# Optimization experiments

Hardware: AMD Instinct MI355X
Metric: run time of the kernel (lower is better)

## Reference

```python
import jax, jax.numpy as jnp
import numpy as np

CLIP_MIN = 0.0  # recurrent_clip_min resolved in build() when -1
CLIP_MAX = 1.0  # recurrent_clip_max default when timesteps unknown


def setup_inputs() -> dict:
    key = jax.random.key(0)
    k1, k2, k3 = jax.random.split(key, 3)
    B, T, D, U = 64, 512, 256, 512
    x = jax.random.normal(k1, (B, T, D), dtype=jnp.float32)
    h0 = jnp.zeros((B, U), dtype=jnp.float32)
    W = jax.random.normal(k2, (D, U), dtype=jnp.float32) * (1.0 / np.sqrt(D))
    u = jax.random.uniform(k3, (U,), dtype=jnp.float32)  # uniform in clip range
    b = jnp.zeros((U,), dtype=jnp.float32)
    return {"x": x, "h0": h0, "W": W, "u": u, "b": b}


def reference(x, h0, W, u, b):
    # IndRNN: h_t = relu(x_t @ W + h_{t-1} * u + b), u clipped to [0, 1]
    u_c = jnp.clip(u, CLIP_MIN, CLIP_MAX)
    # One-time input projection for all timesteps: [B,T,U]
    proj = jnp.einsum("btd,du->btu", x, W) + b
    proj_t = jnp.swapaxes(proj, 0, 1)  # [T,B,U] for scan over time

    def step(h, p_t):
        h_new = jax.nn.relu(p_t + h * u_c)
        return h_new, h_new

    _, hs = jax.lax.scan(step, h0, proj_t)  # hs: [T,B,U]
    return jnp.swapaxes(hs, 0, 1)  # [B,T,U]
```

## Files before the change

kernel.cpp:

```cpp
#include <hip/hip_runtime.h>


__device__ __forceinline__ unsigned short f2bf(float f) {
    unsigned int u = __float_as_uint(f);
    unsigned int r = (u + 0x7FFF + ((u >> 16) & 1)) >> 16;
    return (unsigned short)r;
}

typedef __bf16 bf16x8 __attribute__((ext_vector_type(8)));
typedef float f32x4 __attribute__((ext_vector_type(4)));

typedef const unsigned char __attribute__((address_space(1))) gc_t;
typedef unsigned char __attribute__((address_space(3))) lds_t;

__device__ __forceinline__ void gl_lds16(const void* g, void* l) {
    __builtin_amdgcn_global_load_lds((gc_t*)g, (lds_t*)l, 16, 0, 0);
}

__global__ __launch_bounds__(256) void conv_x(
    const float* __restrict__ x, unsigned short* __restrict__ xb, int n4)
{
    int i = blockIdx.x * blockDim.x + threadIdx.x;
    if (i >= n4) return;
    float4 v = *(const float4*)(x + (long)i * 4);
    ushort4 o;
    o.x = f2bf(v.x); o.y = f2bf(v.y); o.z = f2bf(v.z); o.w = f2bf(v.w);
    *(ushort4*)(xb + (long)i * 4) = o;
}

__global__ __launch_bounds__(256) void conv_wt(
    const float* __restrict__ W, unsigned short* __restrict__ Wt, int K, int N)
{
    int idx = blockIdx.x * blockDim.x + threadIdx.x;
    int kq = K >> 2;
    if (idx >= N * kq) return;
    int n = idx / kq;
    int k4 = (idx - n * kq) * 4;
    ushort4 o;
    o.x = f2bf(W[(long)(k4 + 0) * N + n]);
    o.y = f2bf(W[(long)(k4 + 1) * N + n]);
    o.z = f2bf(W[(long)(k4 + 2) * N + n]);
    o.w = f2bf(W[(long)(k4 + 3) * N + n]);
    *(ushort4*)(Wt + (long)n * K + k4) = o;
}

#define TC 64
#define GN 128

__global__ __launch_bounds__(256, 1) void indrnn_fused(
    const unsigned short* __restrict__ xb,
    const unsigned short* __restrict__ wt,
    const float* __restrict__ bias,
    const float* __restrict__ h0,
    const float* __restrict__ uvec,
    float* __restrict__ out,
    int B, int T, int U)
{
    __shared__ char X[2][TC * 512];

    const int tid  = threadIdx.x;
    const int lane = tid & 63;
    const int w    = tid >> 6;
    const int m    = lane & 15;
    const int quad = lane >> 4;
    const int b    = blockIdx.x;
    const int n0   = blockIdx.y * GN;
    const int tq   = (w >> 1) * 32;
    const int cq   = (w & 1) * 64;

    bf16x8 bfr[4][8];
#pragma unroll
    for (int j = 0; j < 4; ++j)
#pragma unroll
        for (int kt = 0; kt < 8; ++kt)
            bfr[j][kt] = *(const bf16x8*)(
                wt + (long)(n0 + cq + j * 16 + m) * 256 + kt * 32 + quad * 8);

    float bb[4];
#pragma unroll
    for (int j = 0; j < 4; ++j) bb[j] = bias[n0 + cq + j * 16 + m];

    float uc = 0.0f, h = 0.0f;
    if (tid < GN) {
        uc = fminf(fmaxf(uvec[n0 + tid], 0.0f), 1.0f);
        h  = h0[(long)b * U + n0 + tid];
    }

    const unsigned short* xrow = xb + (long)b * T * 256;
    const int p  = lane & 31;
    const int hh = lane >> 5;

#pragma unroll
    for (int i = 0; i < 8; ++i) {
        int blk = i * 4 + w;
        int row = blk * 2 + hh;
        int gp  = p ^ (row & 15);
        gl_lds16(xrow + (long)row * 256 + gp * 8, &X[0][blk * 1024]);
    }

    const int nch = T / TC;
    for (int c = 0; c < nch; ++c) {
        char* Xc = X[c & 1];
        asm volatile("s_waitcnt vmcnt(0)" ::: "memory");
        __builtin_amdgcn_sched_barrier(0);
        __syncthreads();

        f32x4 acc[2][4];
#pragma unroll
        for (int i = 0; i < 2; ++i)
#pragma unroll
            for (int j = 0; j < 4; ++j) acc[i][j] = (f32x4){0.f, 0.f, 0.f, 0.f};

#pragma unroll
        for (int kt = 0; kt < 8; ++kt) {
            const int off = (((kt * 4 + quad) ^ m) * 16);
            bf16x8 a0 = *(const bf16x8*)(Xc + (tq + m) * 512 + off);
            bf16x8 a1 = *(const bf16x8*)(Xc + (tq + 16 + m) * 512 + off);
#pragma unroll
            for (int j = 0; j < 4; ++j) {
                acc[0][j] = __builtin_amdgcn_mfma_f32_16x16x32_bf16(
                    a0, bfr[j][kt], acc[0][j], 0, 0, 0);
                acc[1][j] = __builtin_amdgcn_mfma_f32_16x16x32_bf16(
                    a1, bfr[j][kt], acc[1][j], 0, 0, 0);
            }
        }
        __syncthreads();

        float* pf = (float*)Xc;
#pragma unroll
        for (int i = 0; i < 2; ++i)
#pragma unroll
            for (int j = 0; j < 4; ++j)
#pragma unroll
                for (int r = 0; r < 4; ++r) {
                    int tl  = tq + i * 16 + quad * 4 + r;
                    int col = cq + j * 16 + m;
                    int cs  = col ^ (quad << 4);
                    pf[tl * GN + cs] = acc[i][j][r] + bb[j];
                }
        __syncthreads();

        if (c + 1 < nch) {
            char* Xn = X[(c + 1) & 1];
            const unsigned short* gb = xrow + (long)(c + 1) * TC * 256;
#pragma unroll
            for (int i = 0; i < 8; ++i) {
                int blk = i * 4 + w;
                int row = blk * 2 + hh;
                int gp  = p ^ (row & 15);
                gl_lds16(gb + (long)row * 256 + gp * 8, Xn + blk * 1024);
            }
        }

        if (tid < 128) {
            const float* pfr = (const float*)Xc;
            float* og = out + ((long)b * T + c * TC) * U + n0 + tid;
#pragma unroll 8
            for (int t = 0; t < TC; ++t) {
                float pv = pfr[t * GN + (tid ^ (((t >> 2) & 3) << 4))];
                h = fmaxf(fmaf(h, uc, pv), 0.0f);
                og[(long)t * U] = h;
            }
        }
    }
}

#define BM 128
#define BN 128
#define BK 8

__global__ __launch_bounds__(256) void indrnn_gemm_bias(
    const float* __restrict__ A, const float* __restrict__ Bm,
    const float* __restrict__ bias, float* __restrict__ C,
    int M, int N, int K)
{
    __shared__ float As[BK][BM];
    __shared__ float Bs[BK][BN];
    const int tid = threadIdx.x;
    const int row0 = blockIdx.x * BM, col0 = blockIdx.y * BN;
    const int tx = tid & 15, ty = tid >> 4;
    float acc[8][8];
#pragma unroll
    for (int i = 0; i < 8; ++i)
#pragma unroll
        for (int j = 0; j < 8; ++j) acc[i][j] = 0.0f;
    const int am = tid >> 1, ak = (tid & 1) * 4;
    const int bk = tid >> 5, bn = (tid & 31) * 4;
    const float* Aptr = A + (long)(row0 + am) * K + ak;
    const float* Bptr = Bm + (long)bk * N + col0 + bn;
    for (int kt = 0; kt < K; kt += BK) {
        float4 av = *(const float4*)(Aptr + kt);
        float4 bv = *(const float4*)(Bptr + (long)kt * N);
        As[ak + 0][am] = av.x; As[ak + 1][am] = av.y;
        As[ak + 2][am] = av.z; As[ak + 3][am] = av.w;
        *(float4*)&Bs[bk][bn] = bv;
        __syncthreads();
#pragma unroll
        for (int k = 0; k < BK; ++k) {
            float4 a0 = *(const float4*)&As[k][ty * 4];
            float4 a1 = *(const float4*)&As[k][64 + ty * 4];
            float4 b0 = *(const float4*)&Bs[k][tx * 4];
            float4 b1 = *(const float4*)&Bs[k][64 + tx * 4];
            float a[8] = {a0.x, a0.y, a0.z, a0.w, a1.x, a1.y, a1.z, a1.w};
            float bb2[8] = {b0.x, b0.y, b0.z, b0.w, b1.x, b1.y, b1.z, b1.w};
#pragma unroll
            for (int i = 0; i < 8; ++i)
#pragma unroll
                for (int j = 0; j < 8; ++j)
                    acc[i][j] = fmaf(a[i], bb2[j], acc[i][j]);
        }
        __syncthreads();
    }
    float bb[8];
#pragma unroll
    for (int j = 0; j < 4; ++j) {
        bb[j] = bias[col0 + tx * 4 + j];
        bb[j + 4] = bias[col0 + 64 + tx * 4 + j];
    }
#pragma unroll
    for (int i = 0; i < 8; ++i) {
        const int r = (i < 4) ? (ty * 4 + i) : (64 + ty * 4 + (i - 4));
        float* crow = C + (long)(row0 + r) * N + col0;
        float4 v0 = {acc[i][0] + bb[0], acc[i][1] + bb[1], acc[i][2] + bb[2], acc[i][3] + bb[3]};
        float4 v1 = {acc[i][4] + bb[4], acc[i][5] + bb[5], acc[i][6] + bb[6], acc[i][7] + bb[7]};
        *(float4*)(crow + tx * 4) = v0;
        *(float4*)(crow + 64 + tx * 4) = v1;
    }
}

#define SCAN_UNROLL 32

__global__ __launch_bounds__(256) void indrnn_scan(
    float* __restrict__ out, const float* __restrict__ h0,
    const float* __restrict__ u, int B, int T, int U)
{
    const int idx = blockIdx.x * blockDim.x + threadIdx.x;
    if (idx >= B * U) return;
    const int b = idx / U;
    const int un = idx - b * U;
    const float uc = fminf(fmaxf(u[un], 0.0f), 1.0f);
    float h = h0[(long)b * U + un];
    float* p = out + (long)b * T * U + un;
    for (int t = 0; t < T; t += SCAN_UNROLL) {
        float pv[SCAN_UNROLL];
#pragma unroll
        for (int i = 0; i < SCAN_UNROLL; ++i)
            pv[i] = p[(long)(t + i) * U];
#pragma unroll
        for (int i = 0; i < SCAN_UNROLL; ++i) {
            h = fmaxf(fmaf(h, uc, pv[i]), 0.0f);
            pv[i] = h;
        }
#pragma unroll
        for (int i = 0; i < SCAN_UNROLL; ++i)
            p[(long)(t + i) * U] = pv[i];
    }
}

extern "C" void kernel_launch(void* const* d_in, const int* in_sizes, int n_in,
                              void* d_out, int out_size, void* d_ws, size_t ws_size,
                              hipStream_t stream) {
    const float* x  = (const float*)d_in[0];
    const float* h0 = (const float*)d_in[1];
    const float* W  = (const float*)d_in[2];
    const float* u  = (const float*)d_in[3];
    const float* b  = (const float*)d_in[4];
    float* out = (float*)d_out;

    const int U = in_sizes[3];
    const int B = in_sizes[1] / U;
    const int D = in_sizes[2] / U;
    const int T = in_sizes[0] / (B * D);
    const int M = B * T;

    const size_t xb_bytes = (size_t)M * D * sizeof(unsigned short);
    const size_t wt_bytes = (size_t)U * D * sizeof(unsigned short);
    const bool fused_ok = (D == 256) && (U % GN == 0) && (T % TC == 0) &&
                          (ws_size >= xb_bytes + wt_bytes);

    if (fused_ok) {
        unsigned short* xb = (unsigned short*)d_ws;
        unsigned short* wt = (unsigned short*)((char*)d_ws + xb_bytes);

        const int n4 = (M * D) / 4;
        conv_x<<<(n4 + 255) / 256, 256, 0, stream>>>(x, xb, n4);
        const int nwt = U * (D / 4);
        conv_wt<<<(nwt + 255) / 256, 256, 0, stream>>>(W, wt, D, U);

        dim3 g(B, U / GN);
        indrnn_fused<<<g, 256, 0, stream>>>(xb, wt, b, h0, u, out, B, T, U);
    } else {
        dim3 ggrid(M / BM, U / BN);
        indrnn_gemm_bias<<<ggrid, 256, 0, stream>>>(x, W, b, out, M, U, D);
        const int nthreads = B * U;
        indrnn_scan<<<(nthreads + 255) / 256, 256, 0, stream>>>(out, h0, u, B, T, U);
    }
}
```

Before: 122.1 us.

## Fuse fp32-to-bf16 conversion of x into the recurrent kernel's staging loads

Drops the separate conv_x pass that wrote a bf16 copy of x to workspace. The fused kernel now loads fp32 x straight into registers, converts to bf16 and writes the swizzled tile into LDS. The next chunk's loads are issued before the MFMA loop and stored to LDS after it, so they overlap the compute. This removes one kernel launch and a full write plus reread of the bf16 x buffer. In exchange the kernel reads twice the bytes of x, holds 64 extra registers of prefetch data, and loses the async global-to-LDS path.

```diff
diff --git a/kernel.cpp b/kernel.cpp
--- a/kernel.cpp
+++ b/kernel.cpp
@@ -8,25 +8,8 @@
 }
 
 typedef __bf16 bf16x8 __attribute__((ext_vector_type(8)));
+typedef unsigned short u16x8 __attribute__((ext_vector_type(8)));
 typedef float f32x4 __attribute__((ext_vector_type(4)));
-
-typedef const unsigned char __attribute__((address_space(1))) gc_t;
-typedef unsigned char __attribute__((address_space(3))) lds_t;
-
-__device__ __forceinline__ void gl_lds16(const void* g, void* l) {
-    __builtin_amdgcn_global_load_lds((gc_t*)g, (lds_t*)l, 16, 0, 0);
-}
-
-__global__ __launch_bounds__(256) void conv_x(
-    const float* __restrict__ x, unsigned short* __restrict__ xb, int n4)
-{
-    int i = blockIdx.x * blockDim.x + threadIdx.x;
-    if (i >= n4) return;
-    float4 v = *(const float4*)(x + (long)i * 4);
-    ushort4 o;
-    o.x = f2bf(v.x); o.y = f2bf(v.y); o.z = f2bf(v.z); o.w = f2bf(v.w);
-    *(ushort4*)(xb + (long)i * 4) = o;
-}
 
 __global__ __launch_bounds__(256) void conv_wt(
     const float* __restrict__ W, unsigned short* __restrict__ Wt, int K, int N)
@@ -48,7 +31,7 @@
 #define GN 128
 
 __global__ __launch_bounds__(256, 1) void indrnn_fused(
-    const unsigned short* __restrict__ xb,
+    const float* __restrict__ x,
     const unsigned short* __restrict__ wt,
     const float* __restrict__ bias,
     const float* __restrict__ h0,
@@ -86,24 +69,48 @@
         h  = h0[(long)b * U + n0 + tid];
     }
 
-    const unsigned short* xrow = xb + (long)b * T * 256;
-    const int p  = lane & 31;
-    const int hh = lane >> 5;
-
-#pragma unroll
-    for (int i = 0; i < 8; ++i) {
-        int blk = i * 4 + w;
-        int row = blk * 2 + hh;
-        int gp  = p ^ (row & 15);
-        gl_lds16(xrow + (long)row * 256 + gp * 8, &X[0][blk * 1024]);
+    const float* xbase = x + (long)b * T * 256;
+
+    const int srow = tid >> 5;
+    const int spos = tid & 31;
+
+    {
+        float4 ra[8], rb[8];
+#pragma unroll
+        for (int i = 0; i < 8; ++i) {
+            const float* g = xbase + (srow + 8 * i) * 256 + spos * 8;
+            ra[i] = *(const float4*)g;
+            rb[i] = *(const float4*)(g + 4);
+        }
+#pragma unroll
+        for (int i = 0; i < 8; ++i) {
+            int row = srow + 8 * i;
+            int q   = spos ^ (row & 15);
+            u16x8 o;
+            o[0] = f2bf(ra[i].x); o[1] = f2bf(ra[i].y);
+            o[2] = f2bf(ra[i].z); o[3] = f2bf(ra[i].w);
+            o[4] = f2bf(rb[i].x); o[5] = f2bf(rb[i].y);
+            o[6] = f2bf(rb[i].z); o[7] = f2bf(rb[i].w);
+            *(u16x8*)(&X[0][row * 512 + q * 16]) = o;
+        }
     }
 
     const int nch = T / TC;
     for (int c = 0; c < nch; ++c) {
         char* Xc = X[c & 1];
-        asm volatile("s_waitcnt vmcnt(0)" ::: "memory");
-        __builtin_amdgcn_sched_barrier(0);
-        __syncthreads();
+        __syncthreads();
+
+        float4 ra[8], rb[8];
+        const bool more = (c + 1 < nch);
+        if (more) {
+            const float* gb = xbase + (long)(c + 1) * TC * 256;
+#pragma unroll
+            for (int i = 0; i < 8; ++i) {
+                const float* g = gb + (srow + 8 * i) * 256 + spos * 8;
+                ra[i] = *(const float4*)g;
+                rb[i] = *(const float4*)(g + 4);
+            }
+        }
 
         f32x4 acc[2][4];
 #pragma unroll
@@ -126,6 +133,21 @@
         }
         __syncthreads();
 
+        if (more) {
+            char* Xn = X[(c + 1) & 1];
+#pragma unroll
+            for (int i = 0; i < 8; ++i) {
+                int row = srow + 8 * i;
+                int q   = spos ^ (row & 15);
+                u16x8 o;
+                o[0] = f2bf(ra[i].x); o[1] = f2bf(ra[i].y);
+                o[2] = f2bf(ra[i].z); o[3] = f2bf(ra[i].w);
+                o[4] = f2bf(rb[i].x); o[5] = f2bf(rb[i].y);
+                o[6] = f2bf(rb[i].z); o[7] = f2bf(rb[i].w);
+                *(u16x8*)(Xn + row * 512 + q * 16) = o;
+            }
+        }
+
         float* pf = (float*)Xc;
 #pragma unroll
         for (int i = 0; i < 2; ++i)
@@ -140,19 +162,7 @@
                 }
         __syncthreads();
 
-        if (c + 1 < nch) {
-            char* Xn = X[(c + 1) & 1];
-            const unsigned short* gb = xrow + (long)(c + 1) * TC * 256;
-#pragma unroll
-            for (int i = 0; i < 8; ++i) {
-                int blk = i * 4 + w;
-                int row = blk * 2 + hh;
-                int gp  = p ^ (row & 15);
-                gl_lds16(gb + (long)row * 256 + gp * 8, Xn + blk * 1024);
-            }
-        }
-
-        if (tid < 128) {
+        if (tid < GN) {
             const float* pfr = (const float*)Xc;
             float* og = out + ((long)b * T + c * TC) * U + n0 + tid;
 #pragma unroll 8
@@ -273,22 +283,18 @@
     const int T = in_sizes[0] / (B * D);
     const int M = B * T;
 
-    const size_t xb_bytes = (size_t)M * D * sizeof(unsigned short);
     const size_t wt_bytes = (size_t)U * D * sizeof(unsigned short);
     const bool fused_ok = (D == 256) && (U % GN == 0) && (T % TC == 0) &&
-                          (ws_size >= xb_bytes + wt_bytes);
+                          (ws_size >= wt_bytes);
 
     if (fused_ok) {
-        unsigned short* xb = (unsigned short*)d_ws;
-        unsigned short* wt = (unsigned short*)((char*)d_ws + xb_bytes);
-
-        const int n4 = (M * D) / 4;
-        conv_x<<<(n4 + 255) / 256, 256, 0, stream>>>(x, xb, n4);
+        unsigned short* wt = (unsigned short*)d_ws;
+
         const int nwt = U * (D / 4);
         conv_wt<<<(nwt + 255) / 256, 256, 0, stream>>>(W, wt, D, U);
 
         dim3 g(B, U / GN);
-        indrnn_fused<<<g, 256, 0, stream>>>(xb, wt, b, h0, u, out, B, T, U);
+        indrnn_fused<<<g, 256, 0, stream>>>(x, wt, b, h0, u, out, B, T, U);
     } else {
         dim3 ggrid(M / BM, U / BN);
         indrnn_gemm_bias<<<ggrid, 256, 0, stream>>>(x, W, b, out, M, U, D);
```

Result: slower. 126.1 us (+3.2%).

## Store projection column-major in separate LDS buffer and vectorize scan reads

Applied to the files above, without the earlier changes.

Replaces the double-buffered X tile with a single X buffer plus a dedicated projection buffer laid out column-major with an XOR swizzle. MFMA results are written as 16-byte vectors, and each scan thread bulk-loads its 64 timesteps into registers before running the recurrence. This cuts one barrier per chunk and replaces scalar strided LDS reads with vector reads. The trade-off is that the prefetch of the next X chunk now has to finish before the next chunk's GEMM, so some load/compute overlap may be lost, and the 16 vector loads raise register pressure.

```diff
diff --git a/kernel.cpp b/kernel.cpp
--- a/kernel.cpp
+++ b/kernel.cpp
@@ -56,7 +56,8 @@
     float* __restrict__ out,
     int B, int T, int U)
 {
-    __shared__ char X[2][TC * 512];
+    __shared__ char Xs[TC * 512];
+    __shared__ char Ps[GN * TC * 4];
 
     const int tid  = threadIdx.x;
     const int lane = tid & 63;
@@ -95,16 +96,14 @@
         int blk = i * 4 + w;
         int row = blk * 2 + hh;
         int gp  = p ^ (row & 15);
-        gl_lds16(xrow + (long)row * 256 + gp * 8, &X[0][blk * 1024]);
-    }
+        gl_lds16(xrow + (long)row * 256 + gp * 8, &Xs[blk * 1024]);
+    }
+    asm volatile("s_waitcnt vmcnt(0)" ::: "memory");
+    __builtin_amdgcn_sched_barrier(0);
+    __syncthreads();
 
     const int nch = T / TC;
     for (int c = 0; c < nch; ++c) {
-        char* Xc = X[c & 1];
-        asm volatile("s_waitcnt vmcnt(0)" ::: "memory");
-        __builtin_amdgcn_sched_barrier(0);
-        __syncthreads();
-
         f32x4 acc[2][4];
 #pragma unroll
         for (int i = 0; i < 2; ++i)
@@ -114,8 +113,8 @@
 #pragma unroll
         for (int kt = 0; kt < 8; ++kt) {
             const int off = (((kt * 4 + quad) ^ m) * 16);
-            bf16x8 a0 = *(const bf16x8*)(Xc + (tq + m) * 512 + off);
-            bf16x8 a1 = *(const bf16x8*)(Xc + (tq + 16 + m) * 512 + off);
+            bf16x8 a0 = *(const bf16x8*)(Xs + (tq + m) * 512 + off);
+            bf16x8 a1 = *(const bf16x8*)(Xs + (tq + 16 + m) * 512 + off);
 #pragma unroll
             for (int j = 0; j < 4; ++j) {
                 acc[0][j] = __builtin_amdgcn_mfma_f32_16x16x32_bf16(
@@ -124,44 +123,50 @@
                     a1, bfr[j][kt], acc[1][j], 0, 0, 0);
             }
         }
+
+#pragma unroll
+        for (int i = 0; i < 2; ++i)
+#pragma unroll
+            for (int j = 0; j < 4; ++j) {
+                f32x4 v = acc[i][j];
+                f32x4 vb = {v[0] + bb[j], v[1] + bb[j], v[2] + bb[j], v[3] + bb[j]};
+                int col = cq + j * 16 + m;
+                int g   = (tq >> 2) + i * 4 + quad;
+                *(f32x4*)(Ps + col * 256 + (((g ^ (col & 7)) << 4))) = vb;
+            }
         __syncthreads();
 
-        float* pf = (float*)Xc;
-#pragma unroll
-        for (int i = 0; i < 2; ++i)
-#pragma unroll
-            for (int j = 0; j < 4; ++j)
-#pragma unroll
-                for (int r = 0; r < 4; ++r) {
-                    int tl  = tq + i * 16 + quad * 4 + r;
-                    int col = cq + j * 16 + m;
-                    int cs  = col ^ (quad << 4);
-                    pf[tl * GN + cs] = acc[i][j][r] + bb[j];
-                }
-        __syncthreads();
-
         if (c + 1 < nch) {
-            char* Xn = X[(c + 1) & 1];
             const unsigned short* gb = xrow + (long)(c + 1) * TC * 256;
 #pragma unroll
             for (int i = 0; i < 8; ++i) {
                 int blk = i * 4 + w;
                 int row = blk * 2 + hh;
                 int gp  = p ^ (row & 15);
-                gl_lds16(gb + (long)row * 256 + gp * 8, Xn + blk * 1024);
+                gl_lds16(gb + (long)row * 256 + gp * 8, &Xs[blk * 1024]);
             }
         }
 
-        if (tid < 128) {
-            const float* pfr = (const float*)Xc;
+        if (tid < GN) {
+            f32x4 pv[16];
+            const int ub = tid * 256;
+            const int ux = (tid & 7) << 4;
+#pragma unroll
+            for (int gg = 0; gg < 16; ++gg)
+                pv[gg] = *(const f32x4*)(Ps + ub + ((gg << 4) ^ ux));
             float* og = out + ((long)b * T + c * TC) * U + n0 + tid;
-#pragma unroll 8
-            for (int t = 0; t < TC; ++t) {
-                float pv = pfr[t * GN + (tid ^ (((t >> 2) & 3) << 4))];
-                h = fmaxf(fmaf(h, uc, pv), 0.0f);
-                og[(long)t * U] = h;
-            }
-        }
+#pragma unroll
+            for (int gg = 0; gg < 16; ++gg)
+#pragma unroll
+                for (int e = 0; e < 4; ++e) {
+                    h = fmaxf(fmaf(h, uc, pv[gg][e]), 0.0f);
+                    og[(long)(gg * 4 + e) * U] = h;
+                }
+        }
+
+        asm volatile("s_waitcnt vmcnt(0)" ::: "memory");
+        __builtin_amdgcn_sched_barrier(0);
+        __syncthreads();
     }
 }
 
```

New measurement: 118.7 us. 2.8% less time.
